# Kernel optimization log

Hardware: AMD Instinct MI355X
Metric: run time of the kernel (lower is better)

Reference implementation:

```python
import jax, jax.numpy as jnp
import numpy as np

N_PATHS = 8
T2_EFF = 0.5 * 100.0 + 0.5 * (100 // 50)  # p_dimer*T2_dimer + p_trimer*T2_trimer = 51.0
J_FREQ = 20.0


def setup_inputs() -> dict:
    key = jax.random.key(0)
    ks = jax.random.split(key, 5)
    B, D, H, P = 2048, 1024, 1024, N_PATHS
    return {
        "x": jax.random.normal(ks[0], (B, D), dtype=jnp.float32),
        "W_input": jax.random.normal(ks[1], (D, H), dtype=jnp.float32) * 0.1,
        "W_paths": jax.random.normal(ks[2], (P, H, H), dtype=jnp.float32) * 0.1,
        "J_coupling": jax.random.normal(ks[3], (P, P), dtype=jnp.float32) * 0.01,
        "coherent_state": jax.random.normal(ks[4], (B, P, H), dtype=jnp.float32),
        "t": jnp.ones((1,), dtype=jnp.float32),  # time_since_formation buffer
    }


def reference(x, W_input, W_paths, J_coupling, coherent_state, t):
    # base activation: [B, H]
    base = x @ W_input
    # all per-path matmuls batched into one einsum: [B, P, H]
    path_act = jnp.einsum("bh,phk->bpk", base, W_paths)
    # coherence decay gate (scalar, broadcasts)
    alpha = jnp.clip(jnp.exp(-t[0] / T2_EFF), 0.0, 1.0)
    superposition = alpha * coherent_state + (1.0 - alpha) * path_act
    # interference matrix from symmetrized J-coupling
    J_sym = 0.5 * (J_coupling + J_coupling.T)
    phase = 2.0 * jnp.pi * J_FREQ * t[0] / 1000.0
    interference = jax.nn.softmax(jnp.cos(phase * J_sym), axis=1)  # [P, P]
    # double-loop mixing == small matmul over path dim
    interfered = jnp.einsum("ij,bjh->bih", interference, superposition) / N_PATHS
    interfered = interfered * alpha  # coherence_factor == alpha
    # no measurement (default path): mean over paths
    return jnp.mean(interfered, axis=1)  # [B, H]
```

## Files before the change

### kernel.cpp

```cpp
#include <hip/hip_runtime.h>
#include <cstdint>


typedef __attribute__((ext_vector_type(8))) __bf16 bf16x8;
typedef __attribute__((ext_vector_type(4))) float f32x4;
typedef unsigned short u16;

__device__ __forceinline__ u16 f32_to_bf16_rne(float f) {
  unsigned int u = __float_as_uint(f);
  u += 0x7fffu + ((u >> 16) & 1u);
  return (u16)(u >> 16);
}

__device__ __forceinline__ void wave_scalars(const float* __restrict__ J,
                                             const float* __restrict__ t,
                                             float* w_out, float* alpha_out) {
  const int lane = threadIdx.x & 63;
  float tv = t[0];
  float alpha = fminf(fmaxf(expf(-tv / 51.0f), 0.0f), 1.0f);
  float phase = 2.0f * 3.14159265358979323846f * 20.0f * tv / 1000.0f;
  int i = lane >> 3, j = lane & 7;
  float jsym = 0.5f * (J[i * 8 + j] + J[j * 8 + i]);
  float e = expf(cosf(phase * jsym));
  float rs = e;
  rs += __shfl_xor(rs, 1);
  rs += __shfl_xor(rs, 2);
  rs += __shfl_xor(rs, 4);
  float p = e / rs;
  float cs = p;
  cs += __shfl_xor(cs, 8);
  cs += __shfl_xor(cs, 16);
  cs += __shfl_xor(cs, 32);
  *w_out = alpha * (1.0f / 64.0f) * cs;
  *alpha_out = alpha;
}

__global__ __launch_bounds__(256) void k_prep(
    const float* __restrict__ x, const float* __restrict__ win,
    const float* __restrict__ wp, const float* __restrict__ J,
    const float* __restrict__ t, const float* __restrict__ coh,
    u16* __restrict__ xfrag, u16* __restrict__ winfrag,
    u16* __restrict__ wefrag, float* __restrict__ out) {
  __shared__ __align__(16) char smem[33024];
  const int blk = blockIdx.x;
  const int tid = threadIdx.x;
  const int lane = tid & 63;

  if (blk < 256) {
    float* lt = (float*)smem;
    float wv, alpha;
    wave_scalars(J, t, &wv, &alpha);
    float wLO[8];
#pragma unroll
    for (int p = 0; p < 8; p++)
      wLO[p] = __shfl(wv, (lane & 56) | p) * (1.0f - alpha);
    const int a0 = (blk & 15) * 64;
    const int b0 = (blk >> 4) * 64;
    const int rb = tid >> 4, c = tid & 15;
    f32x4 acc[4];
#pragma unroll
    for (int s = 0; s < 4; s++) acc[s] = (f32x4){0.f, 0.f, 0.f, 0.f};
#pragma unroll
    for (int j = 0; j < 8; j++) {
      const float* base = wp + (size_t)j * 1048576 + b0 + c * 4;
      float wj = wLO[j];
#pragma unroll
      for (int s = 0; s < 4; s++)
        acc[s] += wj * *(const f32x4*)(base + (size_t)(a0 + rb + 16 * s) * 1024);
    }
#pragma unroll
    for (int s = 0; s < 4; s++)
#pragma unroll
      for (int e = 0; e < 4; e++) lt[(rb + 16 * s) * 69 + c * 4 + e] = acc[s][e];
    __syncthreads();
#pragma unroll
    for (int s2 = 0; s2 < 2; s2++) {
      int idx = s2 * 256 + tid;
      int lf = idx & 63, ktl = (idx >> 6) & 1, rtl = idx >> 7;
      int h2l = rtl * 16 + (lf & 15);
      int h1b = ktl * 32 + ((lf >> 4) << 3);
      __align__(16) u16 o[8];
#pragma unroll
      for (int i = 0; i < 8; i++)
        o[i] = f32_to_bf16_rne(lt[(h1b + i) * 69 + h2l]);
      int rt = (b0 >> 4) + rtl, kt = (a0 >> 5) + ktl;
      *(uint4*)(wefrag + ((size_t)(rt * 32 + kt) * 64 + lf) * 8) = *(const uint4*)o;
    }
  } else if (blk < 768) {
    float wv, alpha;
    wave_scalars(J, t, &wv, &alpha);
    float wHI[8];
#pragma unroll
    for (int p = 0; p < 8; p++) wHI[p] = __shfl(wv, (lane & 56) | p) * alpha;
    const f32x4* c4 = (const f32x4*)coh;
    f32x4* o4 = (f32x4*)out;
    const int base = (blk - 256) * 256 + tid;
#pragma unroll
    for (int u = 0; u < 4; u++) {
      int idx = base + u * 131072;
      int b = idx >> 8, hq = idx & 255;
      const f32x4* cb = c4 + (size_t)b * 2048 + hq;
      f32x4 acc = {0.f, 0.f, 0.f, 0.f};
#pragma unroll
      for (int p = 0; p < 8; p++) acc += wHI[p] * cb[p * 256];
      o4[idx] = acc;
    }
  } else {
    const int cid = blk - 768;
    const float* src;
    u16* dst;
    if (cid < 128) {
      src = x + (size_t)cid * 16384;
      dst = xfrag + (size_t)cid * 16384;
    } else {
      src = win + (size_t)(cid - 128) * 16384;
      dst = winfrag + (size_t)(cid - 128) * 16384;
    }
    u16* ld = (u16*)smem;
#pragma unroll
    for (int i = 0; i < 16; i++) {
      int idx = i * 256 + tid;
      int row = idx >> 8, c4i = idx & 255;
      f32x4 v = *(const f32x4*)(src + row * 1024 + c4i * 4);
      ushort4 o;
      o.x = f32_to_bf16_rne(v.x);
      o.y = f32_to_bf16_rne(v.y);
      o.z = f32_to_bf16_rne(v.z);
      o.w = f32_to_bf16_rne(v.w);
      *(ushort4*)(ld + row * 1032 + c4i * 4) = o;
    }
    __syncthreads();
#pragma unroll
    for (int s = 0; s < 8; s++) {
      int idx = s * 256 + tid;
      int lf = idx & 63, kt = idx >> 6;
      int row = lf & 15, colb = kt * 32 + ((lf >> 4) << 3);
      *(uint4*)(dst + (kt * 64 + lf) * 8) = *(const uint4*)(ld + row * 1032 + colb);
    }
  }
}

template <int FM, int RMW>
__global__ __launch_bounds__(256) void k_fgemm(
    const u16* __restrict__ Af, const u16* __restrict__ Bf,
    float* __restrict__ outf, u16* __restrict__ ofrag) {
  const int tid = threadIdx.x;
  const int wave = tid >> 6, lane = tid & 63;
  const int quad = lane >> 4, t16 = lane & 15;
  const int m0 = blockIdx.x * (FM * 32);
  const int n0 = blockIdx.y * 64;
  const int wm = (wave >> 1) * (FM * 16);
  const int wn = (wave & 1) * 32;
  const u16* ap = Af + (size_t)(((m0 + wm) >> 4) * 32) * 512 + lane * 8;
  const u16* bp = Bf + (size_t)(((n0 + wn) >> 4) * 32) * 512 + lane * 8;

  f32x4 acc[FM][2];
#pragma unroll
  for (int mi = 0; mi < FM; mi++)
#pragma unroll
    for (int ni = 0; ni < 2; ni++) acc[mi][ni] = (f32x4){0.f, 0.f, 0.f, 0.f};

#pragma unroll 4
  for (int kt = 0; kt < 32; kt++) {
    bf16x8 a[FM], b[2];
#pragma unroll
    for (int mi = 0; mi < FM; mi++)
      a[mi] = *(const bf16x8*)(ap + (mi * 32 + kt) * 512);
#pragma unroll
    for (int ni = 0; ni < 2; ni++)
      b[ni] = *(const bf16x8*)(bp + (ni * 32 + kt) * 512);
#pragma unroll
    for (int mi = 0; mi < FM; mi++)
#pragma unroll
      for (int ni = 0; ni < 2; ni++)
        acc[mi][ni] = __builtin_amdgcn_mfma_f32_16x16x32_bf16(a[mi], b[ni],
                                                              acc[mi][ni], 0, 0, 0);
  }

  if constexpr (RMW) {
#pragma unroll
    for (int mi = 0; mi < FM; mi++)
#pragma unroll
      for (int r = 0; r < 4; r++) {
        size_t mrow = (size_t)(m0 + wm + mi * 16 + quad * 4 + r) * 1024;
#pragma unroll
        for (int ni = 0; ni < 2; ni++) {
          size_t off = mrow + n0 + wn + ni * 16 + t16;
          outf[off] += acc[mi][ni][r];
        }
      }
  } else {
    __shared__ u16 ct[64 * 72];
#pragma unroll
    for (int mi = 0; mi < FM; mi++)
#pragma unroll
      for (int r = 0; r < 4; r++)
#pragma unroll
        for (int ni = 0; ni < 2; ni++)
          ct[(wm + mi * 16 + quad * 4 + r) * 72 + wn + ni * 16 + t16] =
              f32_to_bf16_rne(acc[mi][ni][r]);
    __syncthreads();
#pragma unroll
    for (int s2 = 0; s2 < 2; s2++) {
      int idx = s2 * 256 + tid;
      int lf = idx & 63, ktl = (idx >> 6) & 1, rtl = idx >> 7;
      int rowl = rtl * 16 + (lf & 15);
      int colb = ktl * 32 + ((lf >> 4) << 3);
      int rt = (m0 >> 4) + rtl, kt = (n0 >> 5) + ktl;
      *(uint4*)(ofrag + ((size_t)(rt * 32 + kt) * 64 + lf) * 8) =
          *(const uint4*)(ct + rowl * 72 + colb);
    }
  }
}

extern "C" void kernel_launch(void* const* d_in, const int* in_sizes, int n_in,
                              void* d_out, int out_size, void* d_ws, size_t ws_size,
                              hipStream_t stream) {
  const float* x   = (const float*)d_in[0];
  const float* win = (const float*)d_in[1];
  const float* wp  = (const float*)d_in[2];
  const float* J   = (const float*)d_in[3];
  const float* coh = (const float*)d_in[4];
  const float* t   = (const float*)d_in[5];
  float* out = (float*)d_out;

  char* ws = (char*)d_ws;
  u16* xfrag   = (u16*)ws;
  u16* winfrag = (u16*)(ws + 4u * 1024 * 1024);
  u16* wefrag  = (u16*)(ws + 6u * 1024 * 1024);
  u16* wctfrag = (u16*)(ws + 8u * 1024 * 1024);

  k_prep<<<960, 256, 0, stream>>>(x, win, wp, J, t, coh, xfrag, winfrag, wefrag,
                                  out);
  k_fgemm<2, 0><<<dim3(16, 16), 256, 0, stream>>>(wefrag, winfrag, nullptr,
                                                  wctfrag);
  k_fgemm<4, 1><<<dim3(16, 16), 256, 0, stream>>>(xfrag, wctfrag, out, nullptr);
}
```

Baseline: 170.1 us.

## Fuse coherent-state mixing into final GEMM with producer waves and retile GEMMs

Moves the coherent-state weighted path reduction out of the prep kernel into the final GEMM kernel. Four extra waves per block compute that contribution into LDS while four waves run the MFMA loop, and the sum is written once instead of written and then read-modify-written. Both GEMMs are retiled to smaller per-block tiles with more blocks, aiming for better CU occupancy on the 256-block grids. The cost is that the coherent-state read now shares blocks with the GEMM and waits behind a block barrier.

```diff
diff --git a/kernel.cpp b/kernel.cpp
--- a/kernel.cpp
+++ b/kernel.cpp
@@ -38,9 +38,8 @@
 __global__ __launch_bounds__(256) void k_prep(
     const float* __restrict__ x, const float* __restrict__ win,
     const float* __restrict__ wp, const float* __restrict__ J,
-    const float* __restrict__ t, const float* __restrict__ coh,
-    u16* __restrict__ xfrag, u16* __restrict__ winfrag,
-    u16* __restrict__ wefrag, float* __restrict__ out) {
+    const float* __restrict__ t, u16* __restrict__ xfrag,
+    u16* __restrict__ winfrag, u16* __restrict__ wefrag) {
   __shared__ __align__(16) char smem[33024];
   const int blk = blockIdx.x;
   const int tid = threadIdx.x;
@@ -86,27 +85,8 @@
       int rt = (b0 >> 4) + rtl, kt = (a0 >> 5) + ktl;
       *(uint4*)(wefrag + ((size_t)(rt * 32 + kt) * 64 + lf) * 8) = *(const uint4*)o;
     }
-  } else if (blk < 768) {
-    float wv, alpha;
-    wave_scalars(J, t, &wv, &alpha);
-    float wHI[8];
-#pragma unroll
-    for (int p = 0; p < 8; p++) wHI[p] = __shfl(wv, (lane & 56) | p) * alpha;
-    const f32x4* c4 = (const f32x4*)coh;
-    f32x4* o4 = (f32x4*)out;
-    const int base = (blk - 256) * 256 + tid;
-#pragma unroll
-    for (int u = 0; u < 4; u++) {
-      int idx = base + u * 131072;
-      int b = idx >> 8, hq = idx & 255;
-      const f32x4* cb = c4 + (size_t)b * 2048 + hq;
-      f32x4 acc = {0.f, 0.f, 0.f, 0.f};
-#pragma unroll
-      for (int p = 0; p < 8; p++) acc += wHI[p] * cb[p * 256];
-      o4[idx] = acc;
-    }
   } else {
-    const int cid = blk - 768;
+    const int cid = blk - 256;
     const float* src;
     u16* dst;
     if (cid < 128) {
@@ -140,76 +120,115 @@
   }
 }
 
-template <int FM, int RMW>
-__global__ __launch_bounds__(256) void k_fgemm(
-    const u16* __restrict__ Af, const u16* __restrict__ Bf,
-    float* __restrict__ outf, u16* __restrict__ ofrag) {
+__global__ __launch_bounds__(256, 4) void k_gemm0(const u16* __restrict__ Af,
+                                                  const u16* __restrict__ Bf,
+                                                  u16* __restrict__ ofrag) {
+  __shared__ u16 ct[64 * 36];
   const int tid = threadIdx.x;
   const int wave = tid >> 6, lane = tid & 63;
   const int quad = lane >> 4, t16 = lane & 15;
-  const int m0 = blockIdx.x * (FM * 32);
-  const int n0 = blockIdx.y * 64;
-  const int wm = (wave >> 1) * (FM * 16);
-  const int wn = (wave & 1) * 32;
-  const u16* ap = Af + (size_t)(((m0 + wm) >> 4) * 32) * 512 + lane * 8;
-  const u16* bp = Bf + (size_t)(((n0 + wn) >> 4) * 32) * 512 + lane * 8;
-
-  f32x4 acc[FM][2];
-#pragma unroll
-  for (int mi = 0; mi < FM; mi++)
-#pragma unroll
-    for (int ni = 0; ni < 2; ni++) acc[mi][ni] = (f32x4){0.f, 0.f, 0.f, 0.f};
-
+  const int m0 = blockIdx.x * 64;
+  const int n0 = blockIdx.y * 32;
+  const u16* ap = Af + ((size_t)((m0 + wave * 16) >> 4) * 32) * 512 + lane * 8;
+  const u16* bp = Bf + ((size_t)(n0 >> 4) * 32) * 512 + lane * 8;
+
+  f32x4 acc[2] = {{0.f, 0.f, 0.f, 0.f}, {0.f, 0.f, 0.f, 0.f}};
 #pragma unroll 4
   for (int kt = 0; kt < 32; kt++) {
-    bf16x8 a[FM], b[2];
-#pragma unroll
-    for (int mi = 0; mi < FM; mi++)
-      a[mi] = *(const bf16x8*)(ap + (mi * 32 + kt) * 512);
+    bf16x8 a = *(const bf16x8*)(ap + kt * 512);
+    bf16x8 b0 = *(const bf16x8*)(bp + kt * 512);
+    bf16x8 b1 = *(const bf16x8*)(bp + (32 + kt) * 512);
+    acc[0] = __builtin_amdgcn_mfma_f32_16x16x32_bf16(a, b0, acc[0], 0, 0, 0);
+    acc[1] = __builtin_amdgcn_mfma_f32_16x16x32_bf16(a, b1, acc[1], 0, 0, 0);
+  }
+#pragma unroll
+  for (int r = 0; r < 4; r++)
 #pragma unroll
     for (int ni = 0; ni < 2; ni++)
-      b[ni] = *(const bf16x8*)(bp + (ni * 32 + kt) * 512);
-#pragma unroll
-    for (int mi = 0; mi < FM; mi++)
-#pragma unroll
-      for (int ni = 0; ni < 2; ni++)
-        acc[mi][ni] = __builtin_amdgcn_mfma_f32_16x16x32_bf16(a[mi], b[ni],
-                                                              acc[mi][ni], 0, 0, 0);
-  }
-
-  if constexpr (RMW) {
-#pragma unroll
-    for (int mi = 0; mi < FM; mi++)
+      ct[(wave * 16 + quad * 4 + r) * 36 + ni * 16 + t16] =
+          f32_to_bf16_rne(acc[ni][r]);
+  __syncthreads();
+  {
+    int lf = tid & 63, rtl = tid >> 6;
+    int rowl = rtl * 16 + (lf & 15);
+    int colb = (lf >> 4) << 3;
+    __align__(16) u16 o[8];
+#pragma unroll
+    for (int i = 0; i < 8; i++) o[i] = ct[rowl * 36 + colb + i];
+    *(uint4*)(ofrag +
+              ((size_t)(((m0 >> 4) + rtl) * 32 + (n0 >> 5)) * 64 + lf) * 8) =
+        *(const uint4*)o;
+  }
+}
+
+__global__ __launch_bounds__(512, 4) void k_main(
+    const u16* __restrict__ Af, const u16* __restrict__ Bf,
+    const float* __restrict__ coh, const float* __restrict__ J,
+    const float* __restrict__ t, float* __restrict__ out) {
+  __shared__ float cs_lds[64 * 68];
+  const int tid = threadIdx.x;
+  const int wave = tid >> 6, lane = tid & 63;
+  const int m0 = blockIdx.x * 64;
+  const int n0 = blockIdx.y * 64;
+  const int quad = lane >> 4, t16 = lane & 15;
+  const int wm = (wave >> 1) * 32, wn = (wave & 1) * 32;
+
+  f32x4 acc[2][2];
+  if (wave < 4) {
+    const u16* ap = Af + ((size_t)((m0 + wm) >> 4) * 32) * 512 + lane * 8;
+    const u16* bp = Bf + ((size_t)((n0 + wn) >> 4) * 32) * 512 + lane * 8;
+#pragma unroll
+    for (int mi = 0; mi < 2; mi++)
+#pragma unroll
+      for (int ni = 0; ni < 2; ni++) acc[mi][ni] = (f32x4){0.f, 0.f, 0.f, 0.f};
+#pragma unroll 4
+    for (int kt = 0; kt < 32; kt++) {
+      bf16x8 a0 = *(const bf16x8*)(ap + kt * 512);
+      bf16x8 a1 = *(const bf16x8*)(ap + (32 + kt) * 512);
+      bf16x8 b0 = *(const bf16x8*)(bp + kt * 512);
+      bf16x8 b1 = *(const bf16x8*)(bp + (32 + kt) * 512);
+      acc[0][0] = __builtin_amdgcn_mfma_f32_16x16x32_bf16(a0, b0, acc[0][0], 0, 0, 0);
+      acc[0][1] = __builtin_amdgcn_mfma_f32_16x16x32_bf16(a0, b1, acc[0][1], 0, 0, 0);
+      acc[1][0] = __builtin_amdgcn_mfma_f32_16x16x32_bf16(a1, b0, acc[1][0], 0, 0, 0);
+      acc[1][1] = __builtin_amdgcn_mfma_f32_16x16x32_bf16(a1, b1, acc[1][1], 0, 0, 0);
+    }
+  } else {
+    float wv, alpha;
+    wave_scalars(J, t, &wv, &alpha);
+    float wHI[8];
+#pragma unroll
+    for (int p = 0; p < 8; p++) wHI[p] = __shfl(wv, (lane & 56) | p) * alpha;
+    const int tc = (wave - 4) * 64 + lane;
+    const int c4 = tc & 15;
+    const int rb = tc >> 4;
+    const float* cb = coh + (size_t)m0 * 8192 + n0 + c4 * 4;
+    f32x4 a4[4];
+#pragma unroll
+    for (int u = 0; u < 4; u++) a4[u] = (f32x4){0.f, 0.f, 0.f, 0.f};
+#pragma unroll
+    for (int u = 0; u < 4; u++) {
+      const float* cr = cb + (size_t)(rb + 16 * u) * 8192;
+#pragma unroll
+      for (int p = 0; p < 8; p++) a4[u] += wHI[p] * *(const f32x4*)(cr + p * 1024);
+    }
+#pragma unroll
+    for (int u = 0; u < 4; u++)
+      *(f32x4*)&cs_lds[(rb + 16 * u) * 68 + c4 * 4] = a4[u];
+  }
+  __syncthreads();
+  if (wave < 4) {
+#pragma unroll
+    for (int mi = 0; mi < 2; mi++)
 #pragma unroll
       for (int r = 0; r < 4; r++) {
-        size_t mrow = (size_t)(m0 + wm + mi * 16 + quad * 4 + r) * 1024;
+        const int ml = wm + mi * 16 + quad * 4 + r;
+        const size_t mrow = (size_t)(m0 + ml) * 1024;
 #pragma unroll
         for (int ni = 0; ni < 2; ni++) {
-          size_t off = mrow + n0 + wn + ni * 16 + t16;
-          outf[off] += acc[mi][ni][r];
+          const int nl = wn + ni * 16 + t16;
+          out[mrow + n0 + nl] = acc[mi][ni][r] + cs_lds[ml * 68 + nl];
         }
       }
-  } else {
-    __shared__ u16 ct[64 * 72];
-#pragma unroll
-    for (int mi = 0; mi < FM; mi++)
-#pragma unroll
-      for (int r = 0; r < 4; r++)
-#pragma unroll
-        for (int ni = 0; ni < 2; ni++)
-          ct[(wm + mi * 16 + quad * 4 + r) * 72 + wn + ni * 16 + t16] =
-              f32_to_bf16_rne(acc[mi][ni][r]);
-    __syncthreads();
-#pragma unroll
-    for (int s2 = 0; s2 < 2; s2++) {
-      int idx = s2 * 256 + tid;
-      int lf = idx & 63, ktl = (idx >> 6) & 1, rtl = idx >> 7;
-      int rowl = rtl * 16 + (lf & 15);
-      int colb = ktl * 32 + ((lf >> 4) << 3);
-      int rt = (m0 >> 4) + rtl, kt = (n0 >> 5) + ktl;
-      *(uint4*)(ofrag + ((size_t)(rt * 32 + kt) * 64 + lf) * 8) =
-          *(const uint4*)(ct + rowl * 72 + colb);
-    }
   }
 }
 
@@ -230,9 +249,7 @@
   u16* wefrag  = (u16*)(ws + 6u * 1024 * 1024);
   u16* wctfrag = (u16*)(ws + 8u * 1024 * 1024);
 
-  k_prep<<<960, 256, 0, stream>>>(x, win, wp, J, t, coh, xfrag, winfrag, wefrag,
-                                  out);
-  k_fgemm<2, 0><<<dim3(16, 16), 256, 0, stream>>>(wefrag, winfrag, nullptr,
-                                                  wctfrag);
-  k_fgemm<4, 1><<<dim3(16, 16), 256, 0, stream>>>(xfrag, wctfrag, out, nullptr);
-}
+  k_prep<<<448, 256, 0, stream>>>(x, win, wp, J, t, xfrag, winfrag, wefrag);
+  k_gemm0<<<dim3(16, 32), 256, 0, stream>>>(wefrag, winfrag, wctfrag);
+  k_main<<<dim3(32, 16), 512, 0, stream>>>(xfrag, wctfrag, coh, J, t, out);
+}
```

After: 166.6 us. -2.0%, faster.
